# Kernel optimization log

Hardware: AMD Instinct MI355X
Metric: run time of the kernel (lower is better)

## Reference

```python
import jax, jax.numpy as jnp
import numpy as np


def segment_softmax(x, seg, num_segments):
    # numerically-stable softmax over graph segments (rows of the sparse matrix)
    m = jax.ops.segment_max(x, seg, num_segments=num_segments)
    e = jnp.exp(x - m[seg])
    s = jax.ops.segment_sum(e, seg, num_segments=num_segments)
    return e / s[seg]


def setup_inputs() -> dict:
    key = jax.random.key(0)
    ks = jax.random.split(key, 12)
    B, N, E, P, H = 256, 51200, 102400, 5, 300
    instruction = jax.random.normal(ks[0], (B, H), dtype=jnp.float32)
    distribution = jax.random.uniform(ks[1], (N,), dtype=jnp.float32)
    node_attrs = jax.random.normal(ks[2], (N, H), dtype=jnp.float32)
    edge_attrs = jax.random.normal(ks[3], (E, H), dtype=jnp.float32)
    node_indices = jnp.sort(jax.random.randint(ks[4], (N,), 0, B)).astype(jnp.int32)
    edge_batch_indices = jax.random.randint(ks[5], (E,), 0, B).astype(jnp.int32)
    edge_indices = jax.random.randint(ks[6], (2, E), 0, N).astype(jnp.int32)
    prop_embeds = jax.random.normal(ks[7], (P, H), dtype=jnp.float32)
    Ws_property = jax.random.uniform(ks[8], (P, H, H), dtype=jnp.float32)
    W_state = jax.random.uniform(ks[9], (H,), dtype=jnp.float32)
    W_relation = jax.random.uniform(ks[10], (H,), dtype=jnp.float32)
    return {"instruction": instruction, "distribution": distribution, "node_attrs": node_attrs,
            "edge_attrs": edge_attrs, "node_indices": node_indices,
            "edge_batch_indices": edge_batch_indices, "edge_indices": edge_indices,
            "prop_embeds": prop_embeds, "Ws_property": Ws_property,
            "W_state": W_state, "W_relation": W_relation}


def reference(instruction, distribution, node_attrs, edge_attrs, node_indices,
              edge_batch_indices, edge_indices, prop_embeds, Ws_property,
              W_state, W_relation):
    B = instruction.shape[0]
    # [B, P] property similarities
    prop_sim = jax.nn.softmax(instruction @ prop_embeds.T, axis=1)
    ps_node = prop_sim[node_indices]            # [N, P]
    instr_node = instruction[node_indices]      # [N, H]
    # per-property transform of node attrs: [N, P-1, H]
    wx = jnp.einsum('phk,nk->nph', Ws_property[:-1], node_attrs)
    node_scores = jax.nn.elu(jnp.sum(ps_node[:, :-1, None] * instr_node[:, None, :] * wx, axis=1))  # [N, H]
    # relation transform of edge attrs: [E, H]
    edge_wx = jnp.einsum('hk,ek->eh', Ws_property[-1], edge_attrs)
    edge_scores = jax.nn.elu(instruction[edge_batch_indices] * edge_wx)  # [E, H]
    # per-graph (segment) softmax over state logits
    state_logits = node_scores @ W_state        # [N]
    next_states = segment_softmax(state_logits, node_indices, B)
    # scatter-add message passing: dst node accumulates distribution[src] * edge_scores
    agg = jnp.zeros_like(node_scores).at[edge_indices[1]].add(
        distribution[edge_indices[0], None] * edge_scores)  # [N, H]
    rel_logits = agg @ W_relation               # [N]
    next_relations = segment_softmax(rel_logits, node_indices, B)
    r = ps_node[:, -1]
    next_distribution = r * next_relations + (1.0 - r) * next_states
    return next_distribution, prop_sim
```

## Files before the change

### kernel.cpp

```cpp
#include <hip/hip_runtime.h>
#include <math.h>

#define H 300
#define PP 5
#define NE 128
#define KC 32
#define NCH 10
#define ROWB 128
#define WTILE (320 * ROWB)
#define WHALF (160 * ROWB)
#define ATILE (NE * ROWB)
#define NTHREADS 256
#define GT 512

using short8 = __attribute__((ext_vector_type(8))) short;
using f32x4  = __attribute__((ext_vector_type(4))) float;

__device__ __forceinline__ float wsum64(float v) {
#pragma unroll
    for (int m = 32; m >= 1; m >>= 1) v += __shfl_xor(v, m, 64);
    return v;
}
__device__ __forceinline__ float wmax64(float v) {
#pragma unroll
    for (int m = 32; m >= 1; m >>= 1) v = fmaxf(v, __shfl_xor(v, m, 64));
    return v;
}
__device__ __forceinline__ float eluf(float x) { return x > 0.f ? x : expm1f(x); }

__device__ __forceinline__ unsigned short f2bf(float x) {
    unsigned int u = __float_as_uint(x);
    unsigned int r = u + 0x7FFF + ((u >> 16) & 1);
    return (unsigned short)(r >> 16);
}
__device__ __forceinline__ float bf2f(unsigned short h) {
    return __uint_as_float(((unsigned int)h) << 16);
}
__device__ __forceinline__ int sw(int r, int kb) {
    return r * ROWB + (kb ^ ((r & 7) << 4));
}
__device__ __forceinline__ void split4_bits(const float* v, uint2& ph, uint2& pl) {
    unsigned short hs[4], ls[4];
#pragma unroll
    for (int i = 0; i < 4; ++i) {
        hs[i] = f2bf(v[i]);
        ls[i] = f2bf(v[i] - bf2f(hs[i]));
    }
    ph = make_uint2((unsigned)hs[0] | ((unsigned)hs[1] << 16),
                    (unsigned)hs[2] | ((unsigned)hs[3] << 16));
    pl = make_uint2((unsigned)ls[0] | ((unsigned)ls[1] << 16),
                    (unsigned)ls[2] | ((unsigned)ls[3] << 16));
}
__device__ __forceinline__ void split4_cvt(const float* v, uint2& ph, uint2& pl) {
    unsigned h01, h23, l01, l23;
    asm("v_cvt_pk_bf16_f32 %0, %1, %2" : "=v"(h01) : "v"(v[0]), "v"(v[1]));
    asm("v_cvt_pk_bf16_f32 %0, %1, %2" : "=v"(h23) : "v"(v[2]), "v"(v[3]));
    float r0 = v[0] - __uint_as_float(h01 << 16);
    float r1 = v[1] - __uint_as_float(h01 & 0xffff0000u);
    float r2 = v[2] - __uint_as_float(h23 << 16);
    float r3 = v[3] - __uint_as_float(h23 & 0xffff0000u);
    asm("v_cvt_pk_bf16_f32 %0, %1, %2" : "=v"(l01) : "v"(r0), "v"(r1));
    asm("v_cvt_pk_bf16_f32 %0, %1, %2" : "=v"(l23) : "v"(r2), "v"(r3));
    ph = make_uint2(h01, h23);
    pl = make_uint2(l01, l23);
}
__device__ __forceinline__ void gload16(const void* g, void* lds) {
    __builtin_amdgcn_global_load_lds(
        (const __attribute__((address_space(1))) unsigned int*)g,
        (__attribute__((address_space(3))) unsigned int*)lds, 16, 0, 0);
}
#define SBAR() __builtin_amdgcn_s_barrier()
#define SCHED() __builtin_amdgcn_sched_barrier(0)
#define WAIT_LGKM() asm volatile("s_waitcnt lgkmcnt(0)" ::: "memory")
#define WAIT_VM0()  asm volatile("s_waitcnt vmcnt(0)" ::: "memory")
#define WAIT_VM4()  asm volatile("s_waitcnt vmcnt(4)" ::: "memory")
#define WAIT_VM5()  asm volatile("s_waitcnt vmcnt(5)" ::: "memory")

__global__ void k_prop_sim(const float* __restrict__ instr,
                           const float* __restrict__ pe,
                           float* __restrict__ prop_sim) {
    int b = blockIdx.x, lane = threadIdx.x;
    float dots[PP];
#pragma unroll
    for (int p = 0; p < PP; ++p) {
        float s = 0.f;
        for (int hh = lane; hh < H; hh += 64) s += instr[b * H + hh] * pe[p * H + hh];
        dots[p] = wsum64(s);
    }
    if (lane == 0) {
        float m = dots[0];
#pragma unroll
        for (int p = 1; p < PP; ++p) m = fmaxf(m, dots[p]);
        float e[PP], s = 0.f;
#pragma unroll
        for (int p = 0; p < PP; ++p) { e[p] = expf(dots[p] - m); s += e[p]; }
        float inv = 1.f / s;
#pragma unroll
        for (int p = 0; p < PP; ++p) prop_sim[b * PP + p] = e[p] * inv;
    }
}

__global__ void k_counts(const int* __restrict__ idx, int* __restrict__ counts, int N) {
    int i = blockIdx.x * blockDim.x + threadIdx.x;
    if (i < N) atomicAdd(&counts[idx[i]], 1);
}

__global__ void k_scan(const int* __restrict__ counts, int* __restrict__ offsets, int B) {
    __shared__ int sh[256];
    int t = threadIdx.x;
    int c = (t < B) ? counts[t] : 0;
    sh[t] = c;
    __syncthreads();
    for (int off = 1; off < 256; off <<= 1) {
        int v = (t >= off) ? sh[t - off] : 0;
        __syncthreads();
        sh[t] += v;
        __syncthreads();
    }
    if (t < B) offsets[t] = sh[t] - c;
    if (t == B - 1) offsets[B] = sh[t];
}

__global__ void k_presplit(const float* __restrict__ W4, char* __restrict__ img) {
    int c = blockIdx.x;
    int idx = blockIdx.y * NTHREADS + threadIdx.x;
    int r = idx >> 3, j = idx & 7;
    int k = c * KC + j * 4;
    float v[4] = {0.f, 0.f, 0.f, 0.f};
    if (r < H && k < H) *(float4*)v = *(const float4*)&W4[(size_t)r * H + k];
    uint2 ph, pl;
    split4_bits(v, ph, pl);
    char* row = img + (size_t)c * WTILE + (size_t)r * ROWB;
    int x = (r & 7) << 4;
    *(uint2*)(row + ((j * 8) ^ x)) = ph;
    *(uint2*)(row + ((64 + j * 8) ^ x)) = pl;
}

__global__ void k_combine(const float* __restrict__ Ws,
                          const float* __restrict__ prop_sim,
                          const float* __restrict__ instr,
                          char* __restrict__ img) {
    int b = blockIdx.x, c = blockIdx.y, t = threadIdx.x;
    float ps0 = prop_sim[b * PP + 0], ps1 = prop_sim[b * PP + 1];
    float ps2 = prop_sim[b * PP + 2], ps3 = prop_sim[b * PP + 3];
    char* tile = img + ((size_t)b * NCH + c) * WTILE;
#pragma unroll
    for (int i = 0; i < 10; ++i) {
        int idx = t + i * NTHREADS;
        int r = idx >> 3, j = idx & 7;
        int k = c * KC + j * 4;
        float cv[4] = {0.f, 0.f, 0.f, 0.f};
        if (r < H && k < H) {
            float insv = instr[(size_t)b * H + r];
            size_t base = (size_t)r * H + k;
            float w0[4], w1[4], w2[4], w3[4];
            *(float4*)w0 = *(const float4*)&Ws[0 * (size_t)H * H + base];
            *(float4*)w1 = *(const float4*)&Ws[1 * (size_t)H * H + base];
            *(float4*)w2 = *(const float4*)&Ws[2 * (size_t)H * H + base];
            *(float4*)w3 = *(const float4*)&Ws[3 * (size_t)H * H + base];
#pragma unroll
            for (int q = 0; q < 4; ++q)
                cv[q] = insv * fmaf(ps0, w0[q], fmaf(ps1, w1[q], fmaf(ps2, w2[q], ps3 * w3[q])));
        }
        uint2 ph, pl;
        split4_bits(cv, ph, pl);
        char* row = tile + (size_t)r * ROWB;
        int x = (r & 7) << 4;
        *(uint2*)(row + ((j * 8) ^ x)) = ph;
        *(uint2*)(row + ((64 + j * 8) ^ x)) = pl;
    }
}

__global__ __launch_bounds__(GT, 2) void k_gemm(
    const float* __restrict__ na, const float* __restrict__ ea,
    const char* __restrict__ Wc_img, const char* __restrict__ Wr_img,
    const float* __restrict__ instr, const float* __restrict__ wstate,
    const float* __restrict__ wrel,
    const int* __restrict__ offsets, const int* __restrict__ eb,
    const int* __restrict__ ei, const float* __restrict__ dist,
    float* __restrict__ slog, float* __restrict__ rlog,
    int N, int E, int nodeVX)
{
    __shared__ __align__(16) char W_t[2][WHALF];
    __shared__ __align__(16) char A_t[2][ATILE];

    int x = blockIdx.x;
    bool isNode = x < nodeVX;
    const float* Asrc;
    const char* Wsrc;
    int base, rowmax, b = 0, hz, nn = NE;
    if (isNode) {
        int gq = x / 48, r = x - gq * 48;
        int k = r >> 3;
        b = gq * 8 + (r & 7);
        int tile = k >> 1;
        hz = k & 1;
        int start = offsets[b], end = offsets[b + 1];
        base = start + tile * NE;
        if (base >= end) return;
        nn = min(NE, end - base);
        rowmax = N - 1;
        Asrc = na;
        Wsrc = Wc_img + (size_t)b * NCH * WTILE + (size_t)hz * WHALF;
    } else {
        int y = x - nodeVX;
        int gq = y / 16, r = y - gq * 16;
        int e = gq * 8 + (r & 7);
        hz = r >> 3;
        base = e * NE;
        rowmax = E - 1;
        Asrc = ea;
        Wsrc = Wr_img + (size_t)hz * WHALF;
    }

    int t = threadIdx.x;
    int w = t >> 6, l = t & 63, lane16 = l & 15, g = l >> 4;
    int wn = w & 3, wh = w >> 2;

    f32x4 acc[5][2];
#pragma unroll
    for (int ht = 0; ht < 5; ++ht)
#pragma unroll
        for (int cg = 0; cg < 2; ++cg) acc[ht][cg] = (f32x4){0.f, 0.f, 0.f, 0.f};

    float4 pa[2];

    auto loadA = [&](int c) {
#pragma unroll
        for (int i = 0; i < 2; ++i) {
            int idx = t + i * GT;
            int r = idx >> 3, j = idx & 7;
            int k = c * KC + j * 4;
            float4 v = {0.f, 0.f, 0.f, 0.f};
            if (k < H) {
                int row = min(base + r, rowmax);
                v = *(const float4*)&Asrc[(size_t)row * H + k];
            }
            pa[i] = v;
        }
    };
    auto storeA = [&](int sel) {
#pragma unroll
        for (int i = 0; i < 2; ++i) {
            int idx = t + i * GT;
            int r = idx >> 3, j = idx & 7;
            float v[4] = {pa[i].x, pa[i].y, pa[i].z, pa[i].w};
            uint2 ph, pl;
            split4_cvt(v, ph, pl);
            *(uint2*)(A_t[sel] + sw(r, j * 8)) = ph;
            *(uint2*)(A_t[sel] + sw(r, 64 + j * 8)) = pl;
        }
    };
    auto gloadW = [&](int c, int sel) {
        const char* src = Wsrc + (size_t)c * WTILE;
        char* dst = W_t[sel];
        int off = w * 1024 + (l << 4);
        gload16(src + off, dst + off);
        gload16(src + 8192 + off, dst + 8192 + off);
        if (w < 4) gload16(src + 16384 + off, dst + 16384 + off);
    };

    loadA(0);
    gloadW(0, 0);
    storeA(0);
    loadA(1);
    gloadW(1, 1);
    SCHED();
    if (w < 4) { WAIT_VM5(); } else { WAIT_VM4(); }
    WAIT_LGKM();
    SBAR();
    SCHED();

    for (int c = 0; c < NCH; ++c) {
        int cur = c & 1;
        short8 bh[2], bl[2];
#pragma unroll
        for (int cg = 0; cg < 2; ++cg) {
            int brow = wn * 32 + cg * 16 + lane16;
            bh[cg] = *(const short8*)(A_t[cur] + sw(brow, g * 16));
            bl[cg] = *(const short8*)(A_t[cur] + sw(brow, 64 + g * 16));
        }
#pragma unroll
        for (int ht = 0; ht < 5; ++ht) {
            int arow = wh * 80 + ht * 16 + lane16;
            short8 ah = *(const short8*)(W_t[cur] + sw(arow, g * 16));
            short8 al = *(const short8*)(W_t[cur] + sw(arow, 64 + g * 16));
#pragma unroll
            for (int cg = 0; cg < 2; ++cg) {
                acc[ht][cg] = __builtin_amdgcn_mfma_f32_16x16x32_bf16(ah, bh[cg], acc[ht][cg], 0, 0, 0);
                acc[ht][cg] = __builtin_amdgcn_mfma_f32_16x16x32_bf16(ah, bl[cg], acc[ht][cg], 0, 0, 0);
                acc[ht][cg] = __builtin_amdgcn_mfma_f32_16x16x32_bf16(al, bh[cg], acc[ht][cg], 0, 0, 0);
            }
        }
        if (c + 1 < NCH) {
            storeA(cur ^ 1);
            if (c + 2 < NCH) loadA(c + 2);
            WAIT_LGKM();
            SBAR();
            SCHED();
            if (c + 2 < NCH) {
                gloadW(c + 2, cur);
                SCHED();
                if (w < 4) { WAIT_VM5(); } else { WAIT_VM4(); }
            } else {
                WAIT_VM0();
            }
            SBAR();
            SCHED();
        }
    }

    if (isNode) {
#pragma unroll
        for (int cg = 0; cg < 2; ++cg) {
            float part = 0.f;
#pragma unroll
            for (int ht = 0; ht < 5; ++ht) {
                int hb = hz * 160 + wh * 80 + ht * 16 + g * 4;
#pragma unroll
                for (int r = 0; r < 4; ++r) {
                    int h = hb + r;
                    if (h < H) part += wstate[h] * eluf(acc[ht][cg][r]);
                }
            }
            part += __shfl_xor(part, 16, 64);
            part += __shfl_xor(part, 32, 64);
            int col = wn * 32 + cg * 16 + lane16;
            if (l < 16 && col < nn) atomicAdd(&slog[base + col], part);
        }
    } else {
#pragma unroll
        for (int cg = 0; cg < 2; ++cg) {
            int e = base + wn * 32 + cg * 16 + lane16;
            int be = eb[e];
            const float* insb = instr + (size_t)be * H;
            float part = 0.f;
#pragma unroll
            for (int ht = 0; ht < 5; ++ht) {
                int hb = hz * 160 + wh * 80 + ht * 16 + g * 4;
#pragma unroll
                for (int r = 0; r < 4; ++r) {
                    int h = hb + r;
                    if (h < H) part += wrel[h] * eluf(insb[h] * acc[ht][cg][r]);
                }
            }
            part += __shfl_xor(part, 16, 64);
            part += __shfl_xor(part, 32, 64);
            if (l < 16) atomicAdd(&rlog[ei[E + e]], dist[ei[e]] * part);
        }
    }
}

__global__ void k_final(const float* __restrict__ slog, const float* __restrict__ rlog,
                        const float* __restrict__ prop_sim, const int* __restrict__ offsets,
                        float* __restrict__ out)
{
    int b = blockIdx.x;
    int s0 = offsets[b], e1 = offsets[b + 1];
    int t = threadIdx.x, wave = t >> 6, lane = t & 63;
    __shared__ float shA[4], shB[4];
    float mS = -3.0e38f, mR = -3.0e38f;
    for (int i = s0 + t; i < e1; i += 256) {
        mS = fmaxf(mS, slog[i]);
        mR = fmaxf(mR, rlog[i]);
    }
    mS = wmax64(mS); mR = wmax64(mR);
    if (lane == 0) { shA[wave] = mS; shB[wave] = mR; }
    __syncthreads();
    mS = fmaxf(fmaxf(shA[0], shA[1]), fmaxf(shA[2], shA[3]));
    mR = fmaxf(fmaxf(shB[0], shB[1]), fmaxf(shB[2], shB[3]));
    __syncthreads();
    float sS = 0.f, sR = 0.f;
    for (int i = s0 + t; i < e1; i += 256) {
        sS += expf(slog[i] - mS);
        sR += expf(rlog[i] - mR);
    }
    sS = wsum64(sS); sR = wsum64(sR);
    if (lane == 0) { shA[wave] = sS; shB[wave] = sR; }
    __syncthreads();
    sS = shA[0] + shA[1] + shA[2] + shA[3];
    sR = shB[0] + shB[1] + shB[2] + shB[3];
    float r = prop_sim[b * PP + (PP - 1)];
    float iS = 1.f / sS, iR = 1.f / sR;
    for (int i = s0 + t; i < e1; i += 256) {
        float ns = expf(slog[i] - mS) * iS;
        float nr = expf(rlog[i] - mR) * iR;
        out[i] = r * nr + (1.f - r) * ns;
    }
}

extern "C" void kernel_launch(void* const* d_in, const int* in_sizes, int n_in,
                              void* d_out, int out_size, void* d_ws, size_t ws_size,
                              hipStream_t stream) {
    (void)n_in; (void)out_size; (void)ws_size;
    const float* instruction  = (const float*)d_in[0];
    const float* distribution = (const float*)d_in[1];
    const float* node_attrs   = (const float*)d_in[2];
    const float* edge_attrs   = (const float*)d_in[3];
    const int*   node_indices = (const int*)d_in[4];
    const int*   edge_batch   = (const int*)d_in[5];
    const int*   edge_indices = (const int*)d_in[6];
    const float* prop_embeds  = (const float*)d_in[7];
    const float* Ws           = (const float*)d_in[8];
    const float* W_state      = (const float*)d_in[9];
    const float* W_rel        = (const float*)d_in[10];

    int B = in_sizes[0] / H;
    int N = in_sizes[1];
    int E = in_sizes[5];

    float* out = (float*)d_out;
    float* prop_sim = out + N;

    float* ws = (float*)d_ws;
    float* state_logits = ws;
    float* rel_logits   = ws + N;
    int*   offsets      = (int*)(ws + 2 * (size_t)N);
    int*   counts       = offsets + (B + 1);
    uintptr_t wsp = (uintptr_t)(counts + B);
    wsp = (wsp + 255) & ~(uintptr_t)255;
    char* Wr_img = (char*)wsp;
    char* Wc_img = Wr_img + (size_t)NCH * WTILE;

    size_t zero_bytes = (size_t)2 * N * sizeof(float) + (size_t)(2 * B + 1) * sizeof(int);
    hipMemsetAsync(d_ws, 0, zero_bytes, stream);

    int nodeVX = 6 * B;
    int edgeVX = (E / NE) * 2;

    k_prop_sim<<<B, 64, 0, stream>>>(instruction, prop_embeds, prop_sim);
    k_presplit<<<dim3(NCH, 10), NTHREADS, 0, stream>>>(Ws + 4 * (size_t)H * H, Wr_img);
    k_counts<<<(N + 255) / 256, 256, 0, stream>>>(node_indices, counts, N);
    k_scan<<<1, 256, 0, stream>>>(counts, offsets, B);
    k_combine<<<dim3(B, NCH), NTHREADS, 0, stream>>>(Ws, prop_sim, instruction, Wc_img);
    k_gemm<<<nodeVX + edgeVX, GT, 0, stream>>>(
        node_attrs, edge_attrs, Wc_img, Wr_img, instruction, W_state, W_rel,
        offsets, edge_batch, edge_indices, distribution,
        state_logits, rel_logits, N, E, nodeVX);
    k_final<<<B, 256, 0, stream>>>(state_logits, rel_logits, prop_sim, offsets, out);
}
```

Baseline: 298.2 us.

## Process two K-chunks per barrier phase in the fused MFMA GEMM loop

Restructures the double-buffered chunk loop so that both LDS buffers are computed back to back. Their weight and activation tiles are then refilled together, which halves the number of barrier phases. Activations for two chunks are prefetched into registers at once. In exchange, the weight tiles for the next pair are now issued and waited on before any compute can overlap them. Much of the global-load latency that the previous rolling prefetch hid may therefore become exposed.

```diff
diff --git a/kernel.cpp b/kernel.cpp
--- a/kernel.cpp
+++ b/kernel.cpp
@@ -74,7 +74,6 @@
 #define WAIT_LGKM() asm volatile("s_waitcnt lgkmcnt(0)" ::: "memory")
 #define WAIT_VM0()  asm volatile("s_waitcnt vmcnt(0)" ::: "memory")
 #define WAIT_VM4()  asm volatile("s_waitcnt vmcnt(4)" ::: "memory")
-#define WAIT_VM5()  asm volatile("s_waitcnt vmcnt(5)" ::: "memory")
 
 __global__ void k_prop_sim(const float* __restrict__ instr,
                            const float* __restrict__ pe,
@@ -223,32 +222,40 @@
 #pragma unroll
         for (int cg = 0; cg < 2; ++cg) acc[ht][cg] = (f32x4){0.f, 0.f, 0.f, 0.f};
 
-    float4 pa[2];
-
-    auto loadA = [&](int c) {
-#pragma unroll
-        for (int i = 0; i < 2; ++i) {
-            int idx = t + i * GT;
-            int r = idx >> 3, j = idx & 7;
-            int k = c * KC + j * 4;
-            float4 v = {0.f, 0.f, 0.f, 0.f};
-            if (k < H) {
-                int row = min(base + r, rowmax);
-                v = *(const float4*)&Asrc[(size_t)row * H + k];
-            }
-            pa[i] = v;
+    float4 pa[4];
+
+    auto loadA2 = [&](int c) {
+#pragma unroll
+        for (int half = 0; half < 2; ++half) {
+            int cc = c + half;
+#pragma unroll
+            for (int i = 0; i < 2; ++i) {
+                int idx = t + i * GT;
+                int r = idx >> 3, j = idx & 7;
+                int k = cc * KC + j * 4;
+                float4 v = {0.f, 0.f, 0.f, 0.f};
+                if (k < H) {
+                    int row = min(base + r, rowmax);
+                    v = *(const float4*)&Asrc[(size_t)row * H + k];
+                }
+                pa[half * 2 + i] = v;
+            }
         }
     };
-    auto storeA = [&](int sel) {
-#pragma unroll
-        for (int i = 0; i < 2; ++i) {
-            int idx = t + i * GT;
-            int r = idx >> 3, j = idx & 7;
-            float v[4] = {pa[i].x, pa[i].y, pa[i].z, pa[i].w};
-            uint2 ph, pl;
-            split4_cvt(v, ph, pl);
-            *(uint2*)(A_t[sel] + sw(r, j * 8)) = ph;
-            *(uint2*)(A_t[sel] + sw(r, 64 + j * 8)) = pl;
+    auto storeA2 = [&]() {
+#pragma unroll
+        for (int half = 0; half < 2; ++half) {
+#pragma unroll
+            for (int i = 0; i < 2; ++i) {
+                int idx = t + i * GT;
+                int r = idx >> 3, j = idx & 7;
+                float v[4] = {pa[half * 2 + i].x, pa[half * 2 + i].y,
+                              pa[half * 2 + i].z, pa[half * 2 + i].w};
+                uint2 ph, pl;
+                split4_cvt(v, ph, pl);
+                *(uint2*)(A_t[half] + sw(r, j * 8)) = ph;
+                *(uint2*)(A_t[half] + sw(r, 64 + j * 8)) = pl;
+            }
         }
     };
     auto gloadW = [&](int c, int sel) {
@@ -259,32 +266,19 @@
         gload16(src + 8192 + off, dst + 8192 + off);
         if (w < 4) gload16(src + 16384 + off, dst + 16384 + off);
     };
-
-    loadA(0);
-    gloadW(0, 0);
-    storeA(0);
-    loadA(1);
-    gloadW(1, 1);
-    SCHED();
-    if (w < 4) { WAIT_VM5(); } else { WAIT_VM4(); }
-    WAIT_LGKM();
-    SBAR();
-    SCHED();
-
-    for (int c = 0; c < NCH; ++c) {
-        int cur = c & 1;
+    auto computeChunk = [&](int sel) {
         short8 bh[2], bl[2];
 #pragma unroll
         for (int cg = 0; cg < 2; ++cg) {
             int brow = wn * 32 + cg * 16 + lane16;
-            bh[cg] = *(const short8*)(A_t[cur] + sw(brow, g * 16));
-            bl[cg] = *(const short8*)(A_t[cur] + sw(brow, 64 + g * 16));
+            bh[cg] = *(const short8*)(A_t[sel] + sw(brow, g * 16));
+            bl[cg] = *(const short8*)(A_t[sel] + sw(brow, 64 + g * 16));
         }
 #pragma unroll
         for (int ht = 0; ht < 5; ++ht) {
             int arow = wh * 80 + ht * 16 + lane16;
-            short8 ah = *(const short8*)(W_t[cur] + sw(arow, g * 16));
-            short8 al = *(const short8*)(W_t[cur] + sw(arow, 64 + g * 16));
+            short8 ah = *(const short8*)(W_t[sel] + sw(arow, g * 16));
+            short8 al = *(const short8*)(W_t[sel] + sw(arow, 64 + g * 16));
 #pragma unroll
             for (int cg = 0; cg < 2; ++cg) {
                 acc[ht][cg] = __builtin_amdgcn_mfma_f32_16x16x32_bf16(ah, bh[cg], acc[ht][cg], 0, 0, 0);
@@ -292,19 +286,38 @@
                 acc[ht][cg] = __builtin_amdgcn_mfma_f32_16x16x32_bf16(al, bh[cg], acc[ht][cg], 0, 0, 0);
             }
         }
-        if (c + 1 < NCH) {
-            storeA(cur ^ 1);
-            if (c + 2 < NCH) loadA(c + 2);
+    };
+
+    loadA2(0);
+    gloadW(0, 0);
+    gloadW(1, 1);
+    storeA2();
+    loadA2(2);
+    SCHED();
+    WAIT_VM4();
+    WAIT_LGKM();
+    SBAR();
+    SCHED();
+
+    for (int i = 0; i < NCH / 2; ++i) {
+        computeChunk(0);
+        computeChunk(1);
+        if (i + 1 < NCH / 2) {
             WAIT_LGKM();
             SBAR();
             SCHED();
-            if (c + 2 < NCH) {
-                gloadW(c + 2, cur);
+            gloadW(2 * i + 2, 0);
+            gloadW(2 * i + 3, 1);
+            storeA2();
+            if (2 * i + 4 < NCH) {
+                loadA2(2 * i + 4);
                 SCHED();
-                if (w < 4) { WAIT_VM5(); } else { WAIT_VM4(); }
+                WAIT_VM4();
             } else {
+                SCHED();
                 WAIT_VM0();
             }
+            WAIT_LGKM();
             SBAR();
             SCHED();
         }
```

Result: no change. 300.4 us (+0.7%).
